# Optimization experiments

Hardware: AMD Instinct MI355X
Metric: run time of the kernel (lower is better)

The kernel has to match this reference:

```python
import jax, jax.numpy as jnp
import numpy as np

N_HEADS = 16


def setup_inputs() -> dict:
    key = jax.random.key(0)
    ks = jax.random.split(key, 8)
    B, S, D = 2, 2048, 2048
    Dh = D // N_HEADS
    w_scale = 1.0 / np.sqrt(D)  # ~xavier scale
    x = jax.random.normal(ks[0], (B, S, D), jnp.float32)
    Wq = jax.random.normal(ks[1], (D, D), jnp.float32) * w_scale
    Wk = jax.random.normal(ks[2], (D, D), jnp.float32) * w_scale
    Wv = jax.random.normal(ks[3], (D, D), jnp.float32) * w_scale
    Wo = jax.random.normal(ks[4], (D, D), jnp.float32) * w_scale
    freqs_cos = jax.random.uniform(ks[5], (S, Dh // 2), jnp.float32)
    freqs_sin = jax.random.uniform(ks[6], (S, Dh // 2), jnp.float32)
    mask = jnp.ones((B, S, S), dtype=bool)
    return {"x": x, "Wq": Wq, "Wk": Wk, "Wv": Wv, "Wo": Wo,
            "freqs_cos": freqs_cos, "freqs_sin": freqs_sin, "mask": mask}


def _rope(t, cos, sin):
    # t: [B, H, S, Dh]; cos/sin: [S, Dh//2]
    tr = t[..., 0::2]
    ti = t[..., 1::2]
    c = cos[None, None]  # [1,1,S,Dh//2]
    s = sin[None, None]
    rr = tr * c - ti * s
    ri = tr * s + ti * c
    return jnp.stack([rr, ri], axis=-1).reshape(t.shape)


def reference(x, Wq, Wk, Wv, Wo, freqs_cos, freqs_sin, mask):
    B, S, D = x.shape
    H = N_HEADS
    Dh = D // H
    scale = 1.0 / np.sqrt(Dh)

    def heads(y):
        return y.reshape(B, S, H, Dh).transpose(0, 2, 1, 3)  # [B,H,S,Dh]

    # torch nn.Linear: y = x @ W^T
    q = heads(x @ Wq.T)
    k = heads(x @ Wk.T)
    v = heads(x @ Wv.T)

    q = _rope(q, freqs_cos[:S], freqs_sin[:S])
    k = _rope(k, freqs_cos[:S], freqs_sin[:S])

    scores = jnp.einsum('bhqd,bhkd->bhqk', q, k) * scale
    scores = jnp.where(mask[:, None], scores, jnp.float32(-1e9))
    attn = jax.nn.softmax(scores, axis=-1)
    ctx = jnp.einsum('bhqk,bhkd->bhqd', attn, v)
    ctx = ctx.transpose(0, 2, 1, 3).reshape(B, S, D)
    return ctx @ Wo.T
```

## Files before the change

kernel.cpp:

```cpp
#include <hip/hip_runtime.h>
#include <hip/hip_bf16.h>
#include <cstdint>
#include <cstddef>


typedef __bf16 bf16x8 __attribute__((ext_vector_type(8)));
typedef float f32x4 __attribute__((ext_vector_type(4)));
typedef float f32x4v __attribute__((ext_vector_type(4)));
typedef short short8v __attribute__((ext_vector_type(8)));
typedef unsigned short ushort4v __attribute__((ext_vector_type(4)));

__device__ __forceinline__ f32x4 mfma16(bf16x8 a, bf16x8 b, f32x4 c) {
  return __builtin_amdgcn_mfma_f32_16x16x32_bf16(a, b, c, 0, 0, 0);
}

__device__ __forceinline__ unsigned short f2bf_bits(float f) {
  union { __hip_bfloat16 h; unsigned short u; } cv;
  cv.h = __float2bfloat16(f);
  return cv.u;
}

__device__ __forceinline__ void gll16(const void* g, void* l) {
  __builtin_amdgcn_global_load_lds((const __attribute__((address_space(1))) void*)g,
                                   (__attribute__((address_space(3))) void*)l,
                                   16, 0, 0);
}

__global__ __launch_bounds__(256) void cvt5_kernel(
    const float* __restrict__ x, const float* __restrict__ Wq,
    const float* __restrict__ Wk, const float* __restrict__ Wv,
    const float* __restrict__ Wo, __hip_bfloat16* __restrict__ xb,
    __hip_bfloat16* __restrict__ Wqb, __hip_bfloat16* __restrict__ Wkb,
    __hip_bfloat16* __restrict__ Wvb, __hip_bfloat16* __restrict__ Wob) {
  const int blk = blockIdx.x;
  const float* src;
  __hip_bfloat16* dst;
  size_t base;
  if (blk < 4096) {
    src = x; dst = xb; base = (size_t)blk * 2048;
  } else {
    const int wsel = (blk - 4096) >> 11;
    const int r = (blk - 4096) & 2047;
    src = (wsel == 0) ? Wq : (wsel == 1) ? Wk : (wsel == 2) ? Wv : Wo;
    dst = (wsel == 0) ? Wqb : (wsel == 1) ? Wkb : (wsel == 2) ? Wvb : Wob;
    base = (size_t)r * 2048;
  }
  const size_t i0 = base + (size_t)threadIdx.x * 8;
  const f32x4v a = *(const f32x4v*)(src + i0);
  const f32x4v b = *(const f32x4v*)(src + i0 + 4);
  ushort4v p0, p1;
  p0.x = f2bf_bits(a.x); p0.y = f2bf_bits(a.y); p0.z = f2bf_bits(a.z); p0.w = f2bf_bits(a.w);
  p1.x = f2bf_bits(b.x); p1.y = f2bf_bits(b.y); p1.z = f2bf_bits(b.z); p1.w = f2bf_bits(b.w);
  *(ushort4v*)((unsigned short*)dst + i0) = p0;
  *(ushort4v*)((unsigned short*)dst + i0 + 4) = p1;
}

__global__ __launch_bounds__(256) void cvt_kernel(const float* __restrict__ src,
                                                  __hip_bfloat16* __restrict__ dst) {
  const size_t i0 = ((size_t)blockIdx.x * 256 + threadIdx.x) * 8;
  const f32x4v a = *(const f32x4v*)(src + i0);
  const f32x4v b = *(const f32x4v*)(src + i0 + 4);
  ushort4v p0, p1;
  p0.x = f2bf_bits(a.x); p0.y = f2bf_bits(a.y); p0.z = f2bf_bits(a.z); p0.w = f2bf_bits(a.w);
  p1.x = f2bf_bits(b.x); p1.y = f2bf_bits(b.y); p1.z = f2bf_bits(b.z); p1.w = f2bf_bits(b.w);
  *(ushort4v*)((unsigned short*)dst + i0) = p0;
  *(ushort4v*)((unsigned short*)dst + i0 + 4) = p1;
}

__device__ __forceinline__ void gemm_tile_bf16(
    const __hip_bfloat16* A, const __hip_bfloat16* B, short* As, short* Bs,
    int m0, int n0, int w, int lane, int quad, int ln, int wm, int wn,
    f32x4 (&acc)[4][4]) {
  constexpr int KD = 2048;
#pragma unroll 1
  for (int k0 = 0; k0 < KD; k0 += 64) {
#pragma unroll
    for (int i = 0; i < 4; ++i) {
      const int c = ((w * 4 + i) << 6) + lane;
      const int row = c >> 3;
      const int pc = c & 7;
      const int lc = pc ^ (row & 7);
      gll16(A + (size_t)(m0 + row) * KD + k0 + lc * 8, As + ((w * 4 + i) << 6) * 8);
      gll16(B + (size_t)(n0 + row) * KD + k0 + lc * 8, Bs + ((w * 4 + i) << 6) * 8);
    }
    __syncthreads();
#pragma unroll
    for (int kk = 0; kk < 2; ++kk) {
      bf16x8 a[4], b[4];
      const int pc = (kk * 4 + quad) ^ (ln & 7);
#pragma unroll
      for (int i = 0; i < 4; ++i)
        a[i] = *(const bf16x8*)(As + (wm * 64 + i * 16 + ln) * 64 + pc * 8);
#pragma unroll
      for (int j = 0; j < 4; ++j)
        b[j] = *(const bf16x8*)(Bs + (wn * 64 + j * 16 + ln) * 64 + pc * 8);
#pragma unroll
      for (int i = 0; i < 4; ++i)
#pragma unroll
        for (int j = 0; j < 4; ++j) acc[i][j] = mfma16(a[i], b[j], acc[i][j]);
    }
    __syncthreads();
  }
}

__device__ __forceinline__ void gemm_tile_f32w(
    const __hip_bfloat16* A, const float* W, short* As, short* Bs,
    int m0, int n0, int w, int lane, int quad, int ln, int wm, int wn,
    f32x4 (&acc)[4][4]) {
  constexpr int KD = 2048;
#pragma unroll 1
  for (int k0 = 0; k0 < KD; k0 += 64) {
#pragma unroll
    for (int i = 0; i < 4; ++i) {
      const int c = ((w * 4 + i) << 6) + lane;
      const int row = c >> 3;
      const int pc = c & 7;
      const int lc = pc ^ (row & 7);
      gll16(A + (size_t)(m0 + row) * KD + k0 + lc * 8, As + ((w * 4 + i) << 6) * 8);
      const float* gp = W + (size_t)(n0 + row) * KD + k0 + lc * 8;
      const f32x4v u0 = *(const f32x4v*)gp;
      const f32x4v u1 = *(const f32x4v*)(gp + 4);
      short8v pk;
      pk.s0 = (short)f2bf_bits(u0.x); pk.s1 = (short)f2bf_bits(u0.y);
      pk.s2 = (short)f2bf_bits(u0.z); pk.s3 = (short)f2bf_bits(u0.w);
      pk.s4 = (short)f2bf_bits(u1.x); pk.s5 = (short)f2bf_bits(u1.y);
      pk.s6 = (short)f2bf_bits(u1.z); pk.s7 = (short)f2bf_bits(u1.w);
      *(short8v*)(Bs + c * 8) = pk;
    }
    __syncthreads();
#pragma unroll
    for (int kk = 0; kk < 2; ++kk) {
      bf16x8 a[4], b[4];
      const int pc = (kk * 4 + quad) ^ (ln & 7);
#pragma unroll
      for (int i = 0; i < 4; ++i)
        a[i] = *(const bf16x8*)(As + (wm * 64 + i * 16 + ln) * 64 + pc * 8);
#pragma unroll
      for (int j = 0; j < 4; ++j)
        b[j] = *(const bf16x8*)(Bs + (wn * 64 + j * 16 + ln) * 64 + pc * 8);
#pragma unroll
      for (int i = 0; i < 4; ++i)
#pragma unroll
        for (int j = 0; j < 4; ++j) acc[i][j] = mfma16(a[i], b[j], acc[i][j]);
    }
    __syncthreads();
  }
}

__device__ __forceinline__ void epi_qk(__hip_bfloat16* C, f32x4 (&acc)[4][4],
                                       int m0, int n0, int wm, int wn, int quad, int ln) {
#pragma unroll
  for (int i = 0; i < 4; ++i)
#pragma unroll
    for (int j = 0; j < 4; ++j) {
      const int col = n0 + wn * 64 + j * 16 + ln;
#pragma unroll
      for (int r = 0; r < 4; ++r) {
        const int row = m0 + wm * 64 + i * 16 + quad * 4 + r;
        C[(size_t)row * 2048 + col] = __float2bfloat16(acc[i][j][r]);
      }
    }
}

__device__ __forceinline__ void epi_vt(__hip_bfloat16* Vtb, f32x4 (&acc)[4][4],
                                       int m0, int n0, int wm, int wn, int quad, int ln) {
#pragma unroll
  for (int i = 0; i < 4; ++i)
#pragma unroll
    for (int j = 0; j < 4; ++j) {
      const int col = n0 + wn * 64 + j * 16 + ln;
      const int row0 = m0 + wm * 64 + i * 16 + quad * 4;
      const int b_ = row0 >> 11, s = row0 & 2047;
      ushort4v pk;
      pk.x = f2bf_bits(acc[i][j][0]);
      pk.y = f2bf_bits(acc[i][j][1]);
      pk.z = f2bf_bits(acc[i][j][2]);
      pk.w = f2bf_bits(acc[i][j][3]);
      *(ushort4v*)(Vtb + (size_t)(b_ * 2048 + col) * 2048 + s) = pk;
    }
}

__global__ __launch_bounds__(256) void gemm_qkv_b(const __hip_bfloat16* __restrict__ xb,
                                                  const __hip_bfloat16* __restrict__ Wqb,
                                                  const __hip_bfloat16* __restrict__ Wkb,
                                                  const __hip_bfloat16* __restrict__ Wvb,
                                                  __hip_bfloat16* __restrict__ Qb,
                                                  __hip_bfloat16* __restrict__ Kb,
                                                  __hip_bfloat16* __restrict__ Vtb) {
  __shared__ __align__(16) short As[128 * 64];
  __shared__ __align__(16) short Bs[128 * 64];
  const int tid = threadIdx.x;
  const int w = tid >> 6, lane = tid & 63;
  const int quad = lane >> 4, ln = lane & 15;
  const int wm = w >> 1, wn = w & 1;
  const int wsel = blockIdx.x >> 4;
  const int n0 = (blockIdx.x & 15) << 7;
  const int m0 = blockIdx.y << 7;
  const __hip_bfloat16* W = (wsel == 0) ? Wqb : (wsel == 1) ? Wkb : Wvb;

  const f32x4 zero = {0.f, 0.f, 0.f, 0.f};
  f32x4 acc[4][4];
#pragma unroll
  for (int i = 0; i < 4; ++i)
#pragma unroll
    for (int j = 0; j < 4; ++j) acc[i][j] = zero;

  gemm_tile_bf16(xb, W, As, Bs, m0, n0, w, lane, quad, ln, wm, wn, acc);

  if (wsel == 0) epi_qk(Qb, acc, m0, n0, wm, wn, quad, ln);
  else if (wsel == 1) epi_qk(Kb, acc, m0, n0, wm, wn, quad, ln);
  else epi_vt(Vtb, acc, m0, n0, wm, wn, quad, ln);
}

__global__ __launch_bounds__(256) void gemm_qkv_f(const __hip_bfloat16* __restrict__ xb,
                                                  const float* __restrict__ Wq,
                                                  const float* __restrict__ Wk,
                                                  const float* __restrict__ Wv,
                                                  __hip_bfloat16* __restrict__ Qb,
                                                  __hip_bfloat16* __restrict__ Kb,
                                                  __hip_bfloat16* __restrict__ Vtb) {
  __shared__ __align__(16) short As[128 * 64];
  __shared__ __align__(16) short Bs[128 * 64];
  const int tid = threadIdx.x;
  const int w = tid >> 6, lane = tid & 63;
  const int quad = lane >> 4, ln = lane & 15;
  const int wm = w >> 1, wn = w & 1;
  const int wsel = blockIdx.x >> 4;
  const int n0 = (blockIdx.x & 15) << 7;
  const int m0 = blockIdx.y << 7;
  const float* W = (wsel == 0) ? Wq : (wsel == 1) ? Wk : Wv;

  const f32x4 zero = {0.f, 0.f, 0.f, 0.f};
  f32x4 acc[4][4];
#pragma unroll
  for (int i = 0; i < 4; ++i)
#pragma unroll
    for (int j = 0; j < 4; ++j) acc[i][j] = zero;

  gemm_tile_f32w(xb, W, As, Bs, m0, n0, w, lane, quad, ln, wm, wn, acc);

  if (wsel == 0) epi_qk(Qb, acc, m0, n0, wm, wn, quad, ln);
  else if (wsel == 1) epi_qk(Kb, acc, m0, n0, wm, wn, quad, ln);
  else epi_vt(Vtb, acc, m0, n0, wm, wn, quad, ln);
}

template <int BF16W>
__global__ __launch_bounds__(256) void gemm_out_k(const __hip_bfloat16* __restrict__ Ctx,
                                                  const void* __restrict__ Wo,
                                                  float* __restrict__ C) {
  __shared__ __align__(16) short As[128 * 64];
  __shared__ __align__(16) short Bs[128 * 64];
  const int tid = threadIdx.x;
  const int w = tid >> 6, lane = tid & 63;
  const int quad = lane >> 4, ln = lane & 15;
  const int wm = w >> 1, wn = w & 1;
  const int n0 = blockIdx.x << 7;
  const int m0 = blockIdx.y << 7;

  const f32x4 zero = {0.f, 0.f, 0.f, 0.f};
  f32x4 acc[4][4];
#pragma unroll
  for (int i = 0; i < 4; ++i)
#pragma unroll
    for (int j = 0; j < 4; ++j) acc[i][j] = zero;

  if (BF16W)
    gemm_tile_bf16(Ctx, (const __hip_bfloat16*)Wo, As, Bs, m0, n0, w, lane, quad, ln, wm, wn, acc);
  else
    gemm_tile_f32w(Ctx, (const float*)Wo, As, Bs, m0, n0, w, lane, quad, ln, wm, wn, acc);

#pragma unroll
  for (int i = 0; i < 4; ++i)
#pragma unroll
    for (int j = 0; j < 4; ++j) {
      const int col = n0 + wn * 64 + j * 16 + ln;
#pragma unroll
      for (int r = 0; r < 4; ++r) {
        const int row = m0 + wm * 64 + i * 16 + quad * 4 + r;
        C[(size_t)row * 2048 + col] = acc[i][j][r];
      }
    }
}

__global__ __launch_bounds__(256) void rope2_kernel(__hip_bfloat16* __restrict__ Qb,
                                                    __hip_bfloat16* __restrict__ Kb,
                                                    const float* __restrict__ FC,
                                                    const float* __restrict__ FS) {
  const int blk = blockIdx.x;
  __hip_bfloat16* T = (blk < 16384) ? Qb : Kb;
  const float scale = (blk < 16384) ? 0.12751741f : 1.0f;
  const int idx = (blk & 16383) * 256 + threadIdx.x;
  const int row = idx >> 10;
  const int p = idx & 1023;
  const int fi = ((row & 2047) << 6) + (p & 63);
  __hip_bfloat162* tp = (__hip_bfloat162*)T + idx;
  __hip_bfloat162 v = *tp;
  const float c = FC[fi];
  const float sn = FS[fi];
  const float tr = __bfloat162float(v.x);
  const float ti = __bfloat162float(v.y);
  __hip_bfloat162 o;
  o.x = __float2bfloat16((tr * c - ti * sn) * scale);
  o.y = __float2bfloat16((tr * sn + ti * c) * scale);
  *tp = o;
}

__global__ __launch_bounds__(512, 1) void attn_kernel(const __hip_bfloat16* __restrict__ Q,
                                                      const __hip_bfloat16* __restrict__ K,
                                                      const __hip_bfloat16* __restrict__ Vt,
                                                      __hip_bfloat16* __restrict__ O) {
  __shared__ __align__(16) short Kb0[64 * 128];
  __shared__ __align__(16) short Kb1[64 * 128];
  __shared__ __align__(16) short Vb0[128 * 64];
  __shared__ __align__(16) short Vb1[128 * 64];
  __shared__ __align__(16) short Pb[8 * 32 * 72];
  const int tid = threadIdx.x;
  const int w = tid >> 6, lane = tid & 63;
  const int quad = lane >> 4, ln = lane & 15;
  const int bh = blockIdx.x;
  const int b = bh >> 4, h = bh & 15;
  const int qr = (blockIdx.y << 8) + w * 32;

  const __hip_bfloat16* Qw = Q + ((size_t)(b * 2048 + qr) * 2048 + h * 128);
  const __hip_bfloat16* Kh = K + ((size_t)(b * 2048) * 2048 + h * 128);
  const __hip_bfloat16* Vh = Vt + (size_t)bh * 128 * 2048;
  short* Pw = Pb + (w * 32) * 72;

  bf16x8 qf[2][4];
#pragma unroll
  for (int t = 0; t < 2; ++t)
#pragma unroll
    for (int ks = 0; ks < 4; ++ks)
      qf[t][ks] = *(const bf16x8*)(Qw + (size_t)(16 * t + ln) * 2048 + 32 * ks + 8 * quad);

  const f32x4 zero = {0.f, 0.f, 0.f, 0.f};
  float m_i[2] = {-INFINITY, -INFINITY}, l_i[2] = {0.f, 0.f};
  f32x4 oacc[2][8];
#pragma unroll
  for (int t = 0; t < 2; ++t)
#pragma unroll
    for (int j = 0; j < 8; ++j) oacc[t][j] = zero;

#define STAGE_KV(KT, KB, VB)                                                     \
  {                                                                              \
    const __hip_bfloat16* Kt_ = Kh + (size_t)((KT) * 64) * 2048;                 \
    _Pragma("unroll")                                                            \
    for (int i_ = 0; i_ < 2; ++i_) {                                             \
      const int c_ = ((i_ * 8 + w) << 6) + lane;                                 \
      const int rowk_ = c_ >> 4, pck_ = c_ & 15;                                 \
      const int lck_ = pck_ ^ (rowk_ & 15);                                      \
      gll16(Kt_ + (size_t)rowk_ * 2048 + lck_ * 8, (KB) + ((i_ * 8 + w) << 6) * 8); \
      const int rowv_ = c_ >> 3, pcv_ = c_ & 7;                                  \
      const int lcv_ = pcv_ ^ (rowv_ & 7);                                       \
      gll16(Vh + (size_t)rowv_ * 2048 + (KT) * 64 + lcv_ * 8, (VB) + ((i_ * 8 + w) << 6) * 8); \
    }                                                                            \
  }

  STAGE_KV(0, Kb0, Vb0);

#pragma unroll 1
  for (int kt = 0; kt < 32; ++kt) {
    __syncthreads();
    const int ktn = (kt + 1) & 31;
    if (kt & 1) { STAGE_KV(ktn, Kb0, Vb0); } else { STAGE_KV(ktn, Kb1, Vb1); }
    const short* Kb_ = (kt & 1) ? Kb1 : Kb0;
    const short* Vb_ = (kt & 1) ? Vb1 : Vb0;

    f32x4 sacc[2][4];
#pragma unroll
    for (int t = 0; t < 2; ++t)
#pragma unroll
      for (int j = 0; j < 4; ++j) sacc[t][j] = zero;
#pragma unroll
    for (int ks = 0; ks < 4; ++ks) {
      bf16x8 kf[4];
      const int pc = (4 * ks + quad) ^ ln;
#pragma unroll
      for (int j = 0; j < 4; ++j)
        kf[j] = *(const bf16x8*)(Kb_ + (16 * j + ln) * 128 + pc * 8);
#pragma unroll
      for (int t = 0; t < 2; ++t)
#pragma unroll
        for (int j = 0; j < 4; ++j) sacc[t][j] = mfma16(kf[j], qf[t][ks], sacc[t][j]);
    }

    float alpha[2];
#pragma unroll
    for (int t = 0; t < 2; ++t) {
      float mx = sacc[t][0][0];
#pragma unroll
      for (int j = 0; j < 4; ++j)
#pragma unroll
        for (int r = 0; r < 4; ++r) mx = fmaxf(mx, sacc[t][j][r]);
      mx = fmaxf(mx, __shfl_xor(mx, 16));
      mx = fmaxf(mx, __shfl_xor(mx, 32));
      const float mn = fmaxf(m_i[t], mx);
      alpha[t] = exp2f(m_i[t] - mn);
      float rs = 0.f;
#pragma unroll
      for (int j = 0; j < 4; ++j) {
#pragma unroll
        for (int r = 0; r < 4; ++r) {
          const float p = exp2f(sacc[t][j][r] - mn);
          sacc[t][j][r] = p;
          rs += p;
        }
      }
      rs += __shfl_xor(rs, 16);
      rs += __shfl_xor(rs, 32);
      l_i[t] = l_i[t] * alpha[t] + rs;
      m_i[t] = mn;
#pragma unroll
      for (int j = 0; j < 8; ++j) oacc[t][j] *= alpha[t];
#pragma unroll
      for (int j = 0; j < 4; ++j) {
        ushort4v pk;
        pk.x = f2bf_bits(sacc[t][j][0]);
        pk.y = f2bf_bits(sacc[t][j][1]);
        pk.z = f2bf_bits(sacc[t][j][2]);
        pk.w = f2bf_bits(sacc[t][j][3]);
        *(ushort4v*)(Pw + (16 * t + ln) * 72 + 16 * j + 4 * quad) = pk;
      }
    }

#pragma unroll
    for (int ksp = 0; ksp < 2; ++ksp) {
      bf16x8 pf[2], vf[8];
      const int pcv = (4 * ksp + quad) ^ (ln & 7);
#pragma unroll
      for (int t = 0; t < 2; ++t)
        pf[t] = *(const bf16x8*)(Pw + (16 * t + ln) * 72 + 32 * ksp + 8 * quad);
#pragma unroll
      for (int jd = 0; jd < 8; ++jd)
        vf[jd] = *(const bf16x8*)(Vb_ + (16 * jd + ln) * 64 + pcv * 8);
#pragma unroll
      for (int t = 0; t < 2; ++t)
#pragma unroll
        for (int jd = 0; jd < 8; ++jd) oacc[t][jd] = mfma16(vf[jd], pf[t], oacc[t][jd]);
    }
  }
#undef STAGE_KV

  __hip_bfloat16* Ob = O + ((size_t)(b * 2048 + qr) * 2048 + h * 128);
#pragma unroll
  for (int t = 0; t < 2; ++t) {
    const float inv = 1.f / l_i[t];
#pragma unroll
    for (int jd = 0; jd < 8; ++jd) {
      ushort4v pk;
      pk.x = f2bf_bits(oacc[t][jd][0] * inv);
      pk.y = f2bf_bits(oacc[t][jd][1] * inv);
      pk.z = f2bf_bits(oacc[t][jd][2] * inv);
      pk.w = f2bf_bits(oacc[t][jd][3] * inv);
      *(ushort4v*)(Ob + (size_t)(16 * t + ln) * 2048 + 16 * jd + 4 * quad) = pk;
    }
  }
}

extern "C" void kernel_launch(void* const* d_in, const int* in_sizes, int n_in,
                              void* d_out, int out_size, void* d_ws, size_t ws_size,
                              hipStream_t stream) {
  (void)in_sizes; (void)n_in; (void)out_size;
  const float* x  = (const float*)d_in[0];
  const float* Wq = (const float*)d_in[1];
  const float* Wk = (const float*)d_in[2];
  const float* Wv = (const float*)d_in[3];
  const float* Wo = (const float*)d_in[4];
  const float* fc = (const float*)d_in[5];
  const float* fs = (const float*)d_in[6];

  char* ws = (char*)d_ws;
  const size_t SZ = (size_t)4096 * 2048 * sizeof(__hip_bfloat16);
  const size_t WSZ = SZ / 2;
  __hip_bfloat16* Qb  = (__hip_bfloat16*)(ws + 0 * SZ);
  __hip_bfloat16* Kb  = (__hip_bfloat16*)(ws + 1 * SZ);
  __hip_bfloat16* Vtb = (__hip_bfloat16*)(ws + 2 * SZ);
  __hip_bfloat16* xb  = (__hip_bfloat16*)(ws + 3 * SZ);
  __hip_bfloat16* Ctx = xb;
  __hip_bfloat16* Wqb = (__hip_bfloat16*)(ws + 4 * SZ);
  __hip_bfloat16* Wkb = (__hip_bfloat16*)(ws + 4 * SZ + 1 * WSZ);
  __hip_bfloat16* Wvb = (__hip_bfloat16*)(ws + 4 * SZ + 2 * WSZ);
  __hip_bfloat16* Wob = (__hip_bfloat16*)(ws + 4 * SZ + 3 * WSZ);
  const bool big_ws = ws_size >= 4 * SZ + 4 * WSZ;

  if (big_ws) {
    cvt5_kernel<<<12288, 256, 0, stream>>>(x, Wq, Wk, Wv, Wo, xb, Wqb, Wkb, Wvb, Wob);
    gemm_qkv_b<<<dim3(48, 32), 256, 0, stream>>>(xb, Wqb, Wkb, Wvb, Qb, Kb, Vtb);
  } else {
    cvt_kernel<<<4096, 256, 0, stream>>>(x, xb);
    gemm_qkv_f<<<dim3(48, 32), 256, 0, stream>>>(xb, Wq, Wk, Wv, Qb, Kb, Vtb);
  }

  rope2_kernel<<<32768, 256, 0, stream>>>(Qb, Kb, fc, fs);

  attn_kernel<<<dim3(32, 8), 512, 0, stream>>>(Qb, Kb, Vtb, Ctx);

  if (big_ws)
    gemm_out_k<1><<<dim3(16, 32), 256, 0, stream>>>(Ctx, Wob, (float*)d_out);
  else
    gemm_out_k<0><<<dim3(16, 32), 256, 0, stream>>>(Ctx, Wo, (float*)d_out);
}
```

Baseline: 425.4 us.

## Rewrite QKV projection GEMM as 256x256 double-buffered pipelined kernel

Replaces the 128x128 single-buffered QKV GEMM with a 512-thread, 256x256-tile kernel. It uses double-buffered LDS, global_load_lds prefetch interleaved into four quarter-phases, vmcnt waits and s_setprio around the MFMA bursts. Block IDs are remapped so neighbouring workgroups share weight and activation tiles in cache. The goal is to hide global load latency and raise MFMA utilisation. Costs are 128KB of LDS per block, high register pressure, and scalar bf16 stores in the Q/K epilogue.

```diff
diff --git a/kernel.cpp b/kernel.cpp
--- a/kernel.cpp
+++ b/kernel.cpp
@@ -131,7 +131,7 @@
 #pragma unroll
     for (int kk = 0; kk < 2; ++kk) {
       bf16x8 a[4], b[4];
-      const int pc = (kk * 4 + quad) ^ (ln & 7);
+      const int pc = (kk * 4 + quad) ^ (ln & 15 & 7);
 #pragma unroll
       for (int i = 0; i < 4; ++i)
         a[i] = *(const bf16x8*)(As + (wm * 64 + i * 16 + ln) * 64 + pc * 8);
@@ -180,36 +180,154 @@
     }
 }
 
-__global__ __launch_bounds__(256) void gemm_qkv_b(const __hip_bfloat16* __restrict__ xb,
-                                                  const __hip_bfloat16* __restrict__ Wqb,
-                                                  const __hip_bfloat16* __restrict__ Wkb,
-                                                  const __hip_bfloat16* __restrict__ Wvb,
-                                                  __hip_bfloat16* __restrict__ Qb,
-                                                  __hip_bfloat16* __restrict__ Kb,
-                                                  __hip_bfloat16* __restrict__ Vtb) {
-  __shared__ __align__(16) short As[128 * 64];
-  __shared__ __align__(16) short Bs[128 * 64];
+__device__ __forceinline__ void stage_Ar(const __hip_bfloat16* A, short* dst,
+                                         int m0, int kt, int mh, int tid) {
+#pragma unroll
+  for (int u = 0; u < 2; ++u) {
+    const int c = u * 512 + tid;
+    const int sub = c >> 3, pc = c & 7;
+    const int row = ((sub >> 6) << 7) + (mh << 6) + (sub & 63);
+    const int lc = pc ^ (sub & 7);
+    gll16(A + (size_t)(m0 + row) * 2048 + (kt << 6) + lc * 8,
+          dst + row * 64 + pc * 8);
+  }
+}
+
+__device__ __forceinline__ void stage_Br(const __hip_bfloat16* B, short* dst,
+                                         int n0, int kt, int nh, int tid) {
+#pragma unroll
+  for (int u = 0; u < 2; ++u) {
+    const int c = u * 512 + tid;
+    const int sub = c >> 3, pc = c & 7;
+    const int row = ((sub >> 5) << 6) + (nh << 5) + (sub & 31);
+    const int lc = pc ^ (sub & 7);
+    gll16(B + (size_t)(n0 + row) * 2048 + (kt << 6) + lc * 8,
+          dst + row * 64 + pc * 8);
+  }
+}
+
+#define VMW4 asm volatile("s_waitcnt vmcnt(4)" ::: "memory")
+
+#define QPHASE(BUF, MH, NH, STAGE, TAIL)                                        \
+  {                                                                             \
+    const short* As_ = As[BUF];                                                 \
+    const short* Bs_ = Bs[BUF];                                                 \
+    bf16x8 af0[4], af1[4], bg0[2], bg1[2];                                      \
+    const int pc0 = quad ^ ln7;                                                 \
+    const int pc1 = (4 + quad) ^ ln7;                                           \
+    _Pragma("unroll") for (int i = 0; i < 4; ++i) {                             \
+      const int r_ = wm128 + ((MH) << 6) + (i << 4) + ln;                       \
+      af0[i] = *(const bf16x8*)(As_ + r_ * 64 + pc0 * 8);                       \
+      af1[i] = *(const bf16x8*)(As_ + r_ * 64 + pc1 * 8);                       \
+    }                                                                           \
+    _Pragma("unroll") for (int j = 0; j < 2; ++j) {                             \
+      const int r_ = wn64 + ((NH) << 5) + (j << 4) + ln;                        \
+      bg0[j] = *(const bf16x8*)(Bs_ + r_ * 64 + pc0 * 8);                       \
+      bg1[j] = *(const bf16x8*)(Bs_ + r_ * 64 + pc1 * 8);                       \
+    }                                                                           \
+    STAGE;                                                                      \
+    __builtin_amdgcn_s_barrier();                                               \
+    __builtin_amdgcn_s_setprio(1);                                              \
+    _Pragma("unroll") for (int i = 0; i < 4; ++i)                               \
+      _Pragma("unroll") for (int j = 0; j < 2; ++j)                             \
+        acc[((MH) << 2) + i][((NH) << 1) + j] =                                 \
+            mfma16(af0[i], bg0[j], acc[((MH) << 2) + i][((NH) << 1) + j]);      \
+    _Pragma("unroll") for (int i = 0; i < 4; ++i)                               \
+      _Pragma("unroll") for (int j = 0; j < 2; ++j)                             \
+        acc[((MH) << 2) + i][((NH) << 1) + j] =                                 \
+            mfma16(af1[i], bg1[j], acc[((MH) << 2) + i][((NH) << 1) + j]);      \
+    __builtin_amdgcn_s_setprio(0);                                              \
+    TAIL;                                                                       \
+    __builtin_amdgcn_s_barrier();                                               \
+  }
+
+__global__ __launch_bounds__(512, 2) void gemm_qkv8(
+    const __hip_bfloat16* __restrict__ xb,
+    const __hip_bfloat16* __restrict__ Wqb,
+    const __hip_bfloat16* __restrict__ Wkb,
+    const __hip_bfloat16* __restrict__ Wvb,
+    __hip_bfloat16* __restrict__ Qb,
+    __hip_bfloat16* __restrict__ Kb,
+    __hip_bfloat16* __restrict__ Vtb) {
+  __shared__ __align__(16) short As[2][256 * 64];
+  __shared__ __align__(16) short Bs[2][256 * 64];
   const int tid = threadIdx.x;
   const int w = tid >> 6, lane = tid & 63;
   const int quad = lane >> 4, ln = lane & 15;
-  const int wm = w >> 1, wn = w & 1;
-  const int wsel = blockIdx.x >> 4;
-  const int n0 = (blockIdx.x & 15) << 7;
-  const int m0 = blockIdx.y << 7;
-  const __hip_bfloat16* W = (wsel == 0) ? Wqb : (wsel == 1) ? Wkb : Wvb;
+  const int ln7 = ln & 7;
+  const int wm128 = (w >> 2) << 7;
+  const int wn64 = (w & 3) << 6;
+
+  const int d = blockIdx.y * 24 + blockIdx.x;
+  const int wid = (d & 7) * 48 + (d >> 3);
+  const int by = wid / 24;
+  const int bx = wid - by * 24;
+  const int wsel = bx >> 3;
+  const int n0 = (bx & 7) << 8;
+  const int m0 = by << 8;
+  const __hip_bfloat16* Bw = (wsel == 0) ? Wqb : (wsel == 1) ? Wkb : Wvb;
 
   const f32x4 zero = {0.f, 0.f, 0.f, 0.f};
-  f32x4 acc[4][4];
-#pragma unroll
-  for (int i = 0; i < 4; ++i)
+  f32x4 acc[8][4];
+#pragma unroll
+  for (int i = 0; i < 8; ++i)
 #pragma unroll
     for (int j = 0; j < 4; ++j) acc[i][j] = zero;
 
-  gemm_tile_bf16(xb, W, As, Bs, m0, n0, w, lane, quad, ln, wm, wn, acc);
-
-  if (wsel == 0) epi_qk(Qb, acc, m0, n0, wm, wn, quad, ln);
-  else if (wsel == 1) epi_qk(Kb, acc, m0, n0, wm, wn, quad, ln);
-  else epi_vt(Vtb, acc, m0, n0, wm, wn, quad, ln);
+  stage_Ar(xb, As[0], m0, 0, 0, tid);
+  stage_Ar(xb, As[0], m0, 0, 1, tid);
+  stage_Br(Bw, Bs[0], n0, 0, 0, tid);
+  stage_Br(Bw, Bs[0], n0, 0, 1, tid);
+  stage_Br(Bw, Bs[1], n0, 1, 0, tid);
+  stage_Ar(xb, As[1], m0, 1, 0, tid);
+  VMW4;
+  __builtin_amdgcn_s_barrier();
+
+#pragma unroll 1
+  for (int it = 0; it < 16; ++it) {
+    const int t1 = 2 * it + 1;
+    const int t0n = (2 * it + 2) & 31;
+    const int t1n = (2 * it + 3) & 31;
+    QPHASE(0, 0, 0, stage_Ar(xb, As[1], m0, t1, 1, tid), );
+    QPHASE(0, 1, 0, stage_Br(Bw, Bs[1], n0, t1, 1, tid), );
+    QPHASE(0, 0, 1, stage_Br(Bw, Bs[0], n0, t0n, 0, tid), );
+    QPHASE(0, 1, 1, stage_Ar(xb, As[0], m0, t0n, 0, tid), VMW4);
+    QPHASE(1, 0, 0, stage_Ar(xb, As[0], m0, t0n, 1, tid), );
+    QPHASE(1, 1, 0, stage_Br(Bw, Bs[0], n0, t0n, 1, tid), );
+    QPHASE(1, 0, 1, stage_Br(Bw, Bs[1], n0, t1n, 0, tid), );
+    QPHASE(1, 1, 1, stage_Ar(xb, As[1], m0, t1n, 0, tid), VMW4);
+  }
+
+  if (wsel < 2) {
+    __hip_bfloat16* C = (wsel == 0) ? Qb : Kb;
+#pragma unroll
+    for (int mi = 0; mi < 8; ++mi) {
+      const int row0 = m0 + wm128 + ((mi >> 2) << 6) + ((mi & 3) << 4) + (quad << 2);
+#pragma unroll
+      for (int nj = 0; nj < 4; ++nj) {
+        const int col = n0 + wn64 + ((nj >> 1) << 5) + ((nj & 1) << 4) + ln;
+#pragma unroll
+        for (int r = 0; r < 4; ++r)
+          C[(size_t)(row0 + r) * 2048 + col] = __float2bfloat16(acc[mi][nj][r]);
+      }
+    }
+  } else {
+#pragma unroll
+    for (int mi = 0; mi < 8; ++mi) {
+      const int row0 = m0 + wm128 + ((mi >> 2) << 6) + ((mi & 3) << 4) + (quad << 2);
+      const int b_ = row0 >> 11, s = row0 & 2047;
+#pragma unroll
+      for (int nj = 0; nj < 4; ++nj) {
+        const int col = n0 + wn64 + ((nj >> 1) << 5) + ((nj & 1) << 4) + ln;
+        ushort4v pk;
+        pk.x = f2bf_bits(acc[mi][nj][0]);
+        pk.y = f2bf_bits(acc[mi][nj][1]);
+        pk.z = f2bf_bits(acc[mi][nj][2]);
+        pk.w = f2bf_bits(acc[mi][nj][3]);
+        *(ushort4v*)(Vtb + (size_t)(b_ * 2048 + col) * 2048 + s) = pk;
+      }
+    }
+  }
 }
 
 __global__ __launch_bounds__(256) void gemm_qkv_f(const __hip_bfloat16* __restrict__ xb,
@@ -485,7 +603,7 @@
 
   if (big_ws) {
     cvt5_kernel<<<12288, 256, 0, stream>>>(x, Wq, Wk, Wv, Wo, xb, Wqb, Wkb, Wvb, Wob);
-    gemm_qkv_b<<<dim3(48, 32), 256, 0, stream>>>(xb, Wqb, Wkb, Wvb, Qb, Kb, Vtb);
+    gemm_qkv8<<<dim3(24, 16), 512, 0, stream>>>(xb, Wqb, Wkb, Wvb, Qb, Kb, Vtb);
   } else {
     cvt_kernel<<<4096, 256, 0, stream>>>(x, xb);
     gemm_qkv_f<<<dim3(48, 32), 256, 0, stream>>>(xb, Wq, Wk, Wv, Qb, Kb, Vtb);
```

Result: slower. 455.4 us (+7.1%).

## Double-buffer LDS tiles in bf16 GEMMs to overlap global loads with MFMA

Applied to the files above, without the earlier changes.

Replaces the single-buffered bf16 GEMM main loop with a ping-pong pair of LDS buffers for A and B. The next K-tile is issued with global_load_lds before the MFMA work on the current tile, and the loop drops from two barriers to one per iteration. This is meant to hide global-load latency behind compute in the QKV and output projections. In exchange, LDS per block doubles to 64KB, which can lower occupancy, and the last iteration issues a redundant wrapped-around prefetch.

```diff
diff --git a/kernel.cpp b/kernel.cpp
--- a/kernel.cpp
+++ b/kernel.cpp
@@ -67,39 +67,51 @@
   *(ushort4v*)((unsigned short*)dst + i0 + 4) = p1;
 }
 
-__device__ __forceinline__ void gemm_tile_bf16(
-    const __hip_bfloat16* A, const __hip_bfloat16* B, short* As, short* Bs,
+__device__ __forceinline__ void stage128(const __hip_bfloat16* A, const __hip_bfloat16* B,
+                                         short* As, short* Bs, int m0, int n0, int k0,
+                                         int w, int lane) {
+#pragma unroll
+  for (int i = 0; i < 4; ++i) {
+    const int c = ((w * 4 + i) << 6) + lane;
+    const int row = c >> 3;
+    const int pc = c & 7;
+    const int lc = pc ^ (row & 7);
+    gll16(A + (size_t)(m0 + row) * 2048 + k0 + lc * 8, As + ((w * 4 + i) << 6) * 8);
+    gll16(B + (size_t)(n0 + row) * 2048 + k0 + lc * 8, Bs + ((w * 4 + i) << 6) * 8);
+  }
+}
+
+__device__ __forceinline__ void gemm_tile_bf16_db(
+    const __hip_bfloat16* A, const __hip_bfloat16* B,
+    short* As0, short* As1, short* Bs0, short* Bs1,
     int m0, int n0, int w, int lane, int quad, int ln, int wm, int wn,
     f32x4 (&acc)[4][4]) {
   constexpr int KD = 2048;
+  stage128(A, B, As0, Bs0, m0, n0, 0, w, lane);
 #pragma unroll 1
   for (int k0 = 0; k0 < KD; k0 += 64) {
-#pragma unroll
-    for (int i = 0; i < 4; ++i) {
-      const int c = ((w * 4 + i) << 6) + lane;
-      const int row = c >> 3;
-      const int pc = c & 7;
-      const int lc = pc ^ (row & 7);
-      gll16(A + (size_t)(m0 + row) * KD + k0 + lc * 8, As + ((w * 4 + i) << 6) * 8);
-      gll16(B + (size_t)(n0 + row) * KD + k0 + lc * 8, Bs + ((w * 4 + i) << 6) * 8);
-    }
     __syncthreads();
+    const int kn = (k0 + 64) & (KD - 1);
+    const int cur = (k0 >> 6) & 1;
+    if (cur) stage128(A, B, As0, Bs0, m0, n0, kn, w, lane);
+    else     stage128(A, B, As1, Bs1, m0, n0, kn, w, lane);
+    const short* Asc = cur ? As1 : As0;
+    const short* Bsc = cur ? Bs1 : Bs0;
 #pragma unroll
     for (int kk = 0; kk < 2; ++kk) {
       bf16x8 a[4], b[4];
       const int pc = (kk * 4 + quad) ^ (ln & 7);
 #pragma unroll
       for (int i = 0; i < 4; ++i)
-        a[i] = *(const bf16x8*)(As + (wm * 64 + i * 16 + ln) * 64 + pc * 8);
+        a[i] = *(const bf16x8*)(Asc + (wm * 64 + i * 16 + ln) * 64 + pc * 8);
 #pragma unroll
       for (int j = 0; j < 4; ++j)
-        b[j] = *(const bf16x8*)(Bs + (wn * 64 + j * 16 + ln) * 64 + pc * 8);
+        b[j] = *(const bf16x8*)(Bsc + (wn * 64 + j * 16 + ln) * 64 + pc * 8);
 #pragma unroll
       for (int i = 0; i < 4; ++i)
 #pragma unroll
         for (int j = 0; j < 4; ++j) acc[i][j] = mfma16(a[i], b[j], acc[i][j]);
     }
-    __syncthreads();
   }
 }
 
@@ -187,8 +199,10 @@
                                                   __hip_bfloat16* __restrict__ Qb,
                                                   __hip_bfloat16* __restrict__ Kb,
                                                   __hip_bfloat16* __restrict__ Vtb) {
-  __shared__ __align__(16) short As[128 * 64];
-  __shared__ __align__(16) short Bs[128 * 64];
+  __shared__ __align__(16) short As0[128 * 64];
+  __shared__ __align__(16) short As1[128 * 64];
+  __shared__ __align__(16) short Bs0[128 * 64];
+  __shared__ __align__(16) short Bs1[128 * 64];
   const int tid = threadIdx.x;
   const int w = tid >> 6, lane = tid & 63;
   const int quad = lane >> 4, ln = lane & 15;
@@ -205,7 +219,7 @@
 #pragma unroll
     for (int j = 0; j < 4; ++j) acc[i][j] = zero;
 
-  gemm_tile_bf16(xb, W, As, Bs, m0, n0, w, lane, quad, ln, wm, wn, acc);
+  gemm_tile_bf16_db(xb, W, As0, As1, Bs0, Bs1, m0, n0, w, lane, quad, ln, wm, wn, acc);
 
   if (wsel == 0) epi_qk(Qb, acc, m0, n0, wm, wn, quad, ln);
   else if (wsel == 1) epi_qk(Kb, acc, m0, n0, wm, wn, quad, ln);
@@ -248,8 +262,10 @@
 __global__ __launch_bounds__(256) void gemm_out_k(const __hip_bfloat16* __restrict__ Ctx,
                                                   const void* __restrict__ Wo,
                                                   float* __restrict__ C) {
-  __shared__ __align__(16) short As[128 * 64];
-  __shared__ __align__(16) short Bs[128 * 64];
+  __shared__ __align__(16) short As0[128 * 64];
+  __shared__ __align__(16) short As1[128 * 64];
+  __shared__ __align__(16) short Bs0[128 * 64];
+  __shared__ __align__(16) short Bs1[128 * 64];
   const int tid = threadIdx.x;
   const int w = tid >> 6, lane = tid & 63;
   const int quad = lane >> 4, ln = lane & 15;
@@ -265,9 +281,10 @@
     for (int j = 0; j < 4; ++j) acc[i][j] = zero;
 
   if (BF16W)
-    gemm_tile_bf16(Ctx, (const __hip_bfloat16*)Wo, As, Bs, m0, n0, w, lane, quad, ln, wm, wn, acc);
+    gemm_tile_bf16_db(Ctx, (const __hip_bfloat16*)Wo, As0, As1, Bs0, Bs1,
+                      m0, n0, w, lane, quad, ln, wm, wn, acc);
   else
-    gemm_tile_f32w(Ctx, (const float*)Wo, As, Bs, m0, n0, w, lane, quad, ln, wm, wn, acc);
+    gemm_tile_f32w(Ctx, (const float*)Wo, As0, Bs0, m0, n0, w, lane, quad, ln, wm, wn, acc);
 
 #pragma unroll
   for (int i = 0; i < 4; ++i)
```

Result: no change. 429.5 us (+1.0%).
